# Performance work log

Hardware: AMD Instinct MI355X
Metric: run time of the kernel (lower is better)

## Reference

```python
import jax, jax.numpy as jnp
import numpy as np

N, D, R, NB, E = 50000, 128, 16, 10, 1600000
DECAY_RATE = 0.1
LN_EPS = 1e-5

def setup_inputs() -> dict:
    key = jax.random.key(0)
    ks = jax.random.split(key, 12)
    x = jax.random.normal(ks[0], (N, D), dtype=jnp.float32)
    edge_index = jax.random.randint(ks[1], (2, E), 0, N, dtype=jnp.int64)
    edge_type = jax.random.randint(ks[2], (E,), 0, R, dtype=jnp.int64)
    edge_time = jax.random.uniform(ks[3], (E,), dtype=jnp.float32)
    s = 1.0 / np.sqrt(D)
    basis = jax.random.normal(ks[4], (NB, D, D), dtype=jnp.float32) * s   # RGCN basis matrices
    comp = jax.random.normal(ks[5], (R, NB), dtype=jnp.float32) * (1.0 / np.sqrt(NB))
    root = jax.random.normal(ks[6], (D, D), dtype=jnp.float32) * s        # RGCN self-loop weight
    bias = jnp.zeros((D,), dtype=jnp.float32)
    tp_w = jax.random.normal(ks[7], (D, D), dtype=jnp.float32) * s        # time_proj
    tp_b = jnp.zeros((D,), dtype=jnp.float32)
    gamma = jnp.ones((D,), dtype=jnp.float32)
    beta = jnp.zeros((D,), dtype=jnp.float32)
    return {"x": x, "edge_index": edge_index, "edge_type": edge_type, "edge_time": edge_time,
            "basis": basis, "comp": comp, "root": root, "bias": bias,
            "tp_w": tp_w, "tp_b": tp_b, "gamma": gamma, "beta": beta}

def reference(x, edge_index, edge_type, edge_time, basis, comp, root, bias, tp_w, tp_b, gamma, beta):
    n, d = x.shape
    r = comp.shape[0]
    src, dst = edge_index[0], edge_index[1]
    # ---- RGCNConv (basis decomposition, per-relation mean aggregation) ----
    W = jnp.einsum('rb,bio->rio', comp, basis)                 # [R, D, D]
    msg = x[src]                                               # [E, D] gather
    seg = dst * r + edge_type                                  # combined (node, relation) segment id
    agg = jax.ops.segment_sum(msg, seg, num_segments=n * r)    # [N*R, D]
    cnt = jax.ops.segment_sum(jnp.ones_like(seg, dtype=x.dtype), seg, num_segments=n * r)
    agg = (agg / jnp.maximum(cnt, 1.0)[:, None]).reshape(n, r, d)  # per-relation mean
    x_rgcn = jnp.einsum('nrd,rdo->no', agg, W) + x @ root + bias
    # ---- exponential time decay weights, normalized to sum 1 ----
    td = edge_time.max() - edge_time
    td = td / (td.max() + 1e-8)
    w = jnp.exp(-DECAY_RATE * td)
    w = w / (w.sum() + 1e-8)
    # ---- time-decay aggregation (sum over relations == single scatter-add) ----
    agg_t = jax.ops.segment_sum(msg * w[:, None], dst, num_segments=n)
    deg = jax.ops.segment_sum(jnp.ones_like(dst, dtype=x.dtype), dst, num_segments=n)
    x_time = agg_t / jnp.clip(deg, 1.0)[:, None]
    # ---- combine, relu, (dropout=identity in eval), layernorm ----
    xc = x_rgcn + x_time @ tp_w + tp_b
    h = jax.nn.relu(xc)
    mu = h.mean(-1, keepdims=True)
    var = ((h - mu) ** 2).mean(-1, keepdims=True)
    return (h - mu) * jax.lax.rsqrt(var + LN_EPS) * gamma + beta
```

## Files before the change

### kernel.cpp

```cpp
#include <hip/hip_runtime.h>
#include <hip/hip_bf16.h>
#include <math.h>

#define NN 50000
#define DD 128
#define RR 16
#define NBASIS 10
#define NE 1600000
#define NSEG (NN * RR)
#define NSLICE 12
#define KTOT (NSLICE * DD)
#define DECAY 0.1f

#define NB_COARSE 782
#define NBLK_S 1024
#define EPB 1563
#define NHC (NB_COARSE * NBLK_S)
#define NPART2 (NHC / 1024)
#define FINE 1024
#define CAP 2560

typedef short bf16x8 __attribute__((ext_vector_type(8)));
typedef float f32x4 __attribute__((ext_vector_type(4)));
typedef float f32x2 __attribute__((ext_vector_type(2)));

__device__ __forceinline__ ushort f2b(float f) {
    unsigned u = __float_as_uint(f);
    unsigned r = (u + 0x7FFFu + ((u >> 16) & 1u)) >> 16;
    return (ushort)r;
}
__device__ __forceinline__ unsigned cvt_pk_bf16(float lo, float hi) {
    unsigned r;
    asm("v_cvt_pk_bf16_f32 %0, %1, %2" : "=v"(r) : "v"(lo), "v"(hi));
    return r;
}


#define XB_ITEMS (NN * (DD / 4))
#define PREP_ITEMS (XB_ITEMS + DD * KTOT)
__global__ __launch_bounds__(256) void k_s1(
    const int* __restrict__ edst, const float* __restrict__ t,
    const float* __restrict__ x, const float* __restrict__ basis,
    const float* __restrict__ root, const float* __restrict__ tp_w,
    unsigned* __restrict__ red, unsigned* __restrict__ Hc,
    ushort* __restrict__ xb, ushort* __restrict__ Bt3)
{
    const int bid = blockIdx.x;
    const int tid = threadIdx.x;
    if (bid < NBLK_S) {
        __shared__ unsigned h[NB_COARSE];
        for (int i = tid; i < NB_COARSE; i += 256) h[i] = 0u;
        __syncthreads();
        const int e0 = bid * EPB;
        const int e1 = (e0 + EPB < NE) ? e0 + EPB : NE;
        for (int e = e0 + tid; e < e1; e += 256) {
            int d = __builtin_nontemporal_load(edst + e);
            atomicAdd(&h[d >> 6], 1u);
        }
        __syncthreads();
        for (int i = tid; i < NB_COARSE; i += 256)
            Hc[i * NBLK_S + bid] = h[i];
        return;
    }
    if (bid < NBLK_S + 256) {
        __shared__ float smx[4], smn[4];
        float mx = 0.0f, mn = 1e30f;
        const int stride = 256 * 256;
        for (int i = (bid - NBLK_S) * 256 + tid; i < NE / 4; i += stride) {
            f32x4 v = __builtin_nontemporal_load(((const f32x4*)t) + i);
            mx = fmaxf(mx, fmaxf(fmaxf(v.x, v.y), fmaxf(v.z, v.w)));
            mn = fminf(mn, fminf(fminf(v.x, v.y), fminf(v.z, v.w)));
        }
        for (int o = 32; o >= 1; o >>= 1) {
            mx = fmaxf(mx, __shfl_down(mx, o, 64));
            mn = fminf(mn, __shfl_down(mn, o, 64));
        }
        if ((tid & 63) == 0) { smx[tid >> 6] = mx; smn[tid >> 6] = mn; }
        __syncthreads();
        if (tid == 0) {
            mx = fmaxf(fmaxf(smx[0], smx[1]), fmaxf(smx[2], smx[3]));
            mn = fminf(fminf(smn[0], smn[1]), fminf(smn[2], smn[3]));
            atomicMax(&red[0], __float_as_uint(mx));
            atomicMax(&red[1], ~__float_as_uint(mn));
        }
        return;
    }
    int idx = (bid - NBLK_S - 256) * 256 + tid;
    if (idx < XB_ITEMS) {
        f32x4 v = ((const f32x4*)x)[idx];
        uint2 o;
        o.x = cvt_pk_bf16(v.x, v.y);
        o.y = cvt_pk_bf16(v.z, v.w);
        ((uint2*)xb)[idx] = o;
        return;
    }
    int bidx = idx - XB_ITEMS;
    if (bidx >= DD * KTOT) return;
    int j = bidx / KTOT, k = bidx - j * KTOT;
    int s = k >> 7, d = k & 127;
    float v;
    if (s < NBASIS) {
        v = basis[(s * DD + d) * DD + j];
    } else if (s == NBASIS) {
        v = tp_w[d * DD + j];
    } else {
        v = root[d * DD + j];
    }
    Bt3[bidx] = f2b(v);
}

__global__ __launch_bounds__(1024) void k_scan1(unsigned* __restrict__ Hc,
                                                unsigned* __restrict__ part) {
    __shared__ unsigned sh[1024];
    int tid = threadIdx.x;
    int i = blockIdx.x * 1024 + tid;
    unsigned v = Hc[i];
    sh[tid] = v;
    __syncthreads();
    for (int off = 1; off < 1024; off <<= 1) {
        unsigned t = (tid >= off) ? sh[tid - off] : 0u;
        __syncthreads();
        sh[tid] += t;
        __syncthreads();
    }
    Hc[i] = sh[tid] - v;
    if (tid == 1023) part[blockIdx.x] = sh[1023];
}

__global__ __launch_bounds__(1024) void k_scan2(unsigned* __restrict__ part) {
    __shared__ unsigned sh[1024];
    int tid = threadIdx.x;
    unsigned v = (tid < NPART2) ? part[tid] : 0u;
    sh[tid] = v;
    __syncthreads();
    for (int off = 1; off < 1024; off <<= 1) {
        unsigned t = (tid >= off) ? sh[tid - off] : 0u;
        __syncthreads();
        sh[tid] += t;
        __syncthreads();
    }
    if (tid < NPART2) part[tid] = sh[tid] - v;
}

__global__ __launch_bounds__(1024) void k_scan3(unsigned* __restrict__ Hc,
                                                const unsigned* __restrict__ part) {
    int i = blockIdx.x * 1024 + threadIdx.x;
    Hc[i] += part[i >> 10];
}

__global__ __launch_bounds__(256) void k_s3(
    const int* __restrict__ esrc, const int* __restrict__ edst,
    const int* __restrict__ etype, const float* __restrict__ etime,
    const unsigned* __restrict__ Hc, unsigned* __restrict__ red,
    unsigned long long* __restrict__ tmp)
{
    __shared__ unsigned cur[NB_COARSE];
    __shared__ float ssum[4];
    const int bid = blockIdx.x;
    const int tid = threadIdx.x;
    for (int i = tid; i < NB_COARSE; i += 256)
        cur[i] = Hc[i * NBLK_S + bid];
    const float tmax = __uint_as_float(red[0]);
    const float tmin = __uint_as_float(~red[1]);
    const float rtd = -DECAY / (tmax - tmin + 1e-8f);
    __syncthreads();
    float s = 0.0f;
    const int e0 = bid * EPB;
    const int e1 = (e0 + EPB < NE) ? e0 + EPB : NE;
    for (int e = e0 + tid; e < e1; e += 256) {
        int d    = __builtin_nontemporal_load(edst + e);
        int ty   = __builtin_nontemporal_load(etype + e);
        int sv   = __builtin_nontemporal_load(esrc + e);
        float tv = __builtin_nontemporal_load(etime + e);
        float w = __expf((tmax - tv) * rtd);
        s += w;
        unsigned seg = (unsigned)(d * RR + ty);
        unsigned pos = atomicAdd(&cur[seg >> 10], 1u);
        unsigned lo = (unsigned)(sv & 0xFFFF) | ((unsigned)f2b(w) << 16);
        __builtin_nontemporal_store(
            ((unsigned long long)seg << 32) | lo, tmp + pos);
    }
    for (int o = 32; o >= 1; o >>= 1) s += __shfl_down(s, o, 64);
    if ((tid & 63) == 0) ssum[tid >> 6] = s;
    __syncthreads();
    if (tid == 0)
        atomicAdd(((float*)red) + 2, ssum[0] + ssum[1] + ssum[2] + ssum[3]);
}

__global__ __launch_bounds__(512) void k_s4(
    const unsigned long long* __restrict__ tmp, const unsigned* __restrict__ Hc,
    unsigned* __restrict__ srcw, unsigned* __restrict__ segptr)
{
    __shared__ unsigned long long recs[CAP];
    __shared__ unsigned hist[FINE];
    __shared__ unsigned excl[FINE];
    __shared__ unsigned curf[FINE];
    __shared__ unsigned sh[512];
    const int b = blockIdx.x;
    const int tid = threadIdx.x;
    const unsigned start = Hc[b * NBLK_S];
    const unsigned end   = (b + 1 < NB_COARSE) ? Hc[(b + 1) * NBLK_S] : (unsigned)NE;
    int n = (int)(end - start);
    if (n > CAP) n = CAP;
    for (int i = tid; i < FINE; i += 512) hist[i] = 0u;
    for (int i = tid; i < n; i += 512) recs[i] = tmp[start + i];
    __syncthreads();
    const unsigned base = (unsigned)b << 10;
    for (int i = tid; i < n; i += 512)
        atomicAdd(&hist[(unsigned)(recs[i] >> 32) - base], 1u);
    __syncthreads();
    unsigned a0 = hist[2 * tid], a1 = hist[2 * tid + 1];
    sh[tid] = a0 + a1;
    __syncthreads();
    for (int off = 1; off < 512; off <<= 1) {
        unsigned t = (tid >= off) ? sh[tid - off] : 0u;
        __syncthreads();
        sh[tid] += t;
        __syncthreads();
    }
    unsigned pe = sh[tid] - (a0 + a1);
    excl[2 * tid] = pe;          curf[2 * tid] = pe;
    excl[2 * tid + 1] = pe + a0; curf[2 * tid + 1] = pe + a0;
    __syncthreads();
    for (int i = tid; i < n; i += 512) {
        unsigned long long r = recs[i];
        unsigned p = atomicAdd(&curf[(unsigned)(r >> 32) - base], 1u);
        srcw[start + p] = (unsigned)r;
    }
    for (int i = tid; i < FINE; i += 512)
        segptr[(size_t)b * FINE + i] = start + excl[i];
}

__global__ __launch_bounds__(256) void k_gather(
    const ushort* __restrict__ xb, const unsigned* __restrict__ srcw,
    const unsigned* __restrict__ segptr, const unsigned* __restrict__ red,
    const float* __restrict__ comp,
    ushort* __restrict__ A2)
{
    const int wave = threadIdx.x >> 6, lane = threadIdx.x & 63;
    int dst0 = blockIdx.x * 4 + wave;
    if (dst0 >= NN) return;
    const int dst = __builtin_amdgcn_readfirstlane(dst0);
    const float sumw = ((const float*)red)[2];
    const unsigned s0 = (unsigned)dst * RR;
    const unsigned start = segptr[s0];
    const unsigned endAll = segptr[s0 + RR];
    const unsigned deg = endAll - start;
    unsigned* arow = (unsigned*)(A2 + (size_t)dst * KTOT);
    const unsigned* xbu = (const unsigned*)xb;

    f32x2 cb[NBASIS];
#pragma unroll
    for (int b = 0; b < NBASIS; ++b) cb[b] = (f32x2){0.f, 0.f};
    f32x2 acc = {0.f, 0.f}, xt = {0.f, 0.f};

    int r = 0;
    unsigned scur = start;
    unsigned endr = segptr[s0 + 1];
    unsigned e = start;

#define FLUSH_REL {                                                          \
        float scl = (endr > scur) ? (1.0f / (float)(endr - scur)) : 0.0f;    \
        f32x2 t = acc * scl;                                                 \
        _Pragma("unroll")                                                    \
        for (int b = 0; b < NBASIS; ++b)                                     \
            cb[b] += t * comp[r * NBASIS + b];                               \
        acc = (f32x2){0.f, 0.f}; scur = endr; ++r;                           \
        endr = (r < RR) ? segptr[s0 + r + 1] : 0xFFFFFFFFu; }

#define ACCUM(recq, pvq) {                                                   \
        float wgt = __uint_as_float((recq) & 0xFFFF0000u);                   \
        f32x2 v;                                                             \
        v.x = __uint_as_float((pvq) << 16);                                  \
        v.y = __uint_as_float((pvq) & 0xFFFF0000u);                          \
        acc += v;                                                            \
        xt += v * wgt; }

    while (e < endAll) {
        unsigned idx = e + (unsigned)lane;
        unsigned recv = srcw[(idx < endAll) ? idx : (endAll - 1u)];
        unsigned chunk = endAll - e;
        if (chunk > 64u) chunk = 64u;
        unsigned j = 0;
        for (; j + 8u <= chunk; j += 8u) {
            unsigned rec0 = (unsigned)__builtin_amdgcn_readlane((int)recv, (int)(j + 0));
            unsigned rec1 = (unsigned)__builtin_amdgcn_readlane((int)recv, (int)(j + 1));
            unsigned rec2 = (unsigned)__builtin_amdgcn_readlane((int)recv, (int)(j + 2));
            unsigned rec3 = (unsigned)__builtin_amdgcn_readlane((int)recv, (int)(j + 3));
            unsigned rec4 = (unsigned)__builtin_amdgcn_readlane((int)recv, (int)(j + 4));
            unsigned rec5 = (unsigned)__builtin_amdgcn_readlane((int)recv, (int)(j + 5));
            unsigned rec6 = (unsigned)__builtin_amdgcn_readlane((int)recv, (int)(j + 6));
            unsigned rec7 = (unsigned)__builtin_amdgcn_readlane((int)recv, (int)(j + 7));
            unsigned pv0 = xbu[((rec0 & 0xFFFFu) << 6) + lane];
            unsigned pv1 = xbu[((rec1 & 0xFFFFu) << 6) + lane];
            unsigned pv2 = xbu[((rec2 & 0xFFFFu) << 6) + lane];
            unsigned pv3 = xbu[((rec3 & 0xFFFFu) << 6) + lane];
            unsigned pv4 = xbu[((rec4 & 0xFFFFu) << 6) + lane];
            unsigned pv5 = xbu[((rec5 & 0xFFFFu) << 6) + lane];
            unsigned pv6 = xbu[((rec6 & 0xFFFFu) << 6) + lane];
            unsigned pv7 = xbu[((rec7 & 0xFFFFu) << 6) + lane];
            while (e >= endr) FLUSH_REL; ACCUM(rec0, pv0); ++e;
            while (e >= endr) FLUSH_REL; ACCUM(rec1, pv1); ++e;
            while (e >= endr) FLUSH_REL; ACCUM(rec2, pv2); ++e;
            while (e >= endr) FLUSH_REL; ACCUM(rec3, pv3); ++e;
            while (e >= endr) FLUSH_REL; ACCUM(rec4, pv4); ++e;
            while (e >= endr) FLUSH_REL; ACCUM(rec5, pv5); ++e;
            while (e >= endr) FLUSH_REL; ACCUM(rec6, pv6); ++e;
            while (e >= endr) FLUSH_REL; ACCUM(rec7, pv7); ++e;
        }
        for (; j < chunk; ++j) {
            unsigned rc = (unsigned)__builtin_amdgcn_readlane((int)recv, (int)j);
            unsigned pv = xbu[((rc & 0xFFFFu) << 6) + lane];
            while (e >= endr) FLUSH_REL;
            ACCUM(rc, pv);
            ++e;
        }
    }
    while (r < RR) FLUSH_REL;

#pragma unroll
    for (int b = 0; b < NBASIS; ++b)
        __builtin_nontemporal_store(cvt_pk_bf16(cb[b].x, cb[b].y),
                                    arow + b * 64 + lane);

    float s2 = 1.0f / ((sumw + 1e-8f) * fmaxf((float)deg, 1.0f));
    __builtin_nontemporal_store(cvt_pk_bf16(xt.x * s2, xt.y * s2),
                                arow + NBASIS * 64 + lane);
    __builtin_nontemporal_store(
        ((const unsigned*)(xb + (size_t)dst * DD))[lane],
        arow + (NBASIS + 1) * 64 + lane);
#undef FLUSH_REL
#undef ACCUM
}

__global__ __launch_bounds__(256) void k_fgemm(
    const ushort* __restrict__ A2, const ushort* __restrict__ Bt3,
    const float* __restrict__ bias, const float* __restrict__ tpb,
    const float* __restrict__ gamma, const float* __restrict__ beta,
    float* __restrict__ out)
{
    __shared__ unsigned Bs[2][4096];

    const int tid = threadIdx.x;
    const int w = tid >> 6, lane = tid & 63;
    const int quad = lane >> 4, l16 = lane & 15;
    const int n0 = blockIdx.x * 64;

    f32x4 acc[8];
#pragma unroll
    for (int ct = 0; ct < 8; ++ct) acc[ct] = (f32x4){0.f, 0.f, 0.f, 0.f};

    const ushort* arow = A2 + (size_t)(n0 + w * 16 + l16) * KTOT + quad * 8;
    const int srow = lane >> 3;
    const int sc   = lane & 7;

#define STAGE(buf, itv) {                                                    \
        const int k0_ = (itv) * 64;                                          \
        _Pragma("unroll")                                                    \
        for (int i_ = 0; i_ < 4; ++i_) {                                     \
            const int cid_ = i_ * 4 + w;                                     \
            const int row_ = cid_ * 8 + srow;                                \
            const int ck_  = sc ^ (row_ & 7);                                \
            const ushort* gb_ = Bt3 + (size_t)row_ * KTOT + k0_ + ck_ * 8;   \
            __builtin_amdgcn_global_load_lds(                                \
                (const __attribute__((address_space(1))) unsigned*)gb_,      \
                (__attribute__((address_space(3))) unsigned*)&Bs[buf][cid_ * 256], \
                16, 0, 0);                                                   \
        } }

#define COMPUTE(af0_, af1_, Bp_) {                                           \
        _Pragma("unroll")                                                    \
        for (int ct = 0; ct < 8; ++ct) {                                     \
            const int rB = ct * 16 + l16;                                    \
            bf16x8 b0 = *(const bf16x8*)&Bp_[rB * 32 + ((quad ^ (rB & 7)) << 2)];      \
            bf16x8 b1 = *(const bf16x8*)&Bp_[rB * 32 + (((4 + quad) ^ (rB & 7)) << 2)];\
            acc[ct] = __builtin_amdgcn_mfma_f32_16x16x32_bf16(af0_, b0, acc[ct], 0, 0, 0); \
            acc[ct] = __builtin_amdgcn_mfma_f32_16x16x32_bf16(af1_, b1, acc[ct], 0, 0, 0); \
        } }

    STAGE(0, 0);
    bf16x8 a0A = __builtin_nontemporal_load((const bf16x8*)(arow));
    bf16x8 a1A = __builtin_nontemporal_load((const bf16x8*)(arow + 32));
    bf16x8 a0B = __builtin_nontemporal_load((const bf16x8*)(arow + 64));
    bf16x8 a1B = __builtin_nontemporal_load((const bf16x8*)(arow + 96));
    __syncthreads();

    const int NIT = KTOT / 64;
    for (int it = 0; it < NIT; it += 2) {
        STAGE(1, it + 1);
        {
            bf16x8 af0 = a0A, af1 = a1A;
            if (it + 2 < NIT) {
                a0A = __builtin_nontemporal_load((const bf16x8*)(arow + (it + 2) * 64));
                a1A = __builtin_nontemporal_load((const bf16x8*)(arow + (it + 2) * 64 + 32));
            }
            const unsigned* Bp = &Bs[0][0];
            COMPUTE(af0, af1, Bp);
        }
        __syncthreads();
        if (it + 2 < NIT) STAGE(0, it + 2);
        {
            bf16x8 af0 = a0B, af1 = a1B;
            if (it + 3 < NIT) {
                a0B = __builtin_nontemporal_load((const bf16x8*)(arow + (it + 3) * 64));
                a1B = __builtin_nontemporal_load((const bf16x8*)(arow + (it + 3) * 64 + 32));
            }
            const unsigned* Bp = &Bs[1][0];
            COMPUTE(af0, af1, Bp);
        }
        __syncthreads();
    }
#undef STAGE
#undef COMPUTE

    float bc[8], gc[8], be[8];
#pragma unroll
    for (int ct = 0; ct < 8; ++ct) {
        int col = ct * 16 + l16;
        bc[ct] = bias[col] + tpb[col];
        gc[ct] = gamma[col];
        be[ct] = beta[col];
    }
    float s[4] = {0, 0, 0, 0}, q[4] = {0, 0, 0, 0};
#pragma unroll
    for (int ct = 0; ct < 8; ++ct)
#pragma unroll
        for (int i = 0; i < 4; ++i) {
            float v = fmaxf(acc[ct][i] + bc[ct], 0.0f);
            acc[ct][i] = v;
            s[i] += v;
            q[i] = fmaf(v, v, q[i]);
        }
#pragma unroll
    for (int off = 1; off < 16; off <<= 1)
#pragma unroll
        for (int i = 0; i < 4; ++i) {
            s[i] += __shfl_xor(s[i], off, 64);
            q[i] += __shfl_xor(q[i], off, 64);
        }
#pragma unroll
    for (int i = 0; i < 4; ++i) {
        const int row = n0 + w * 16 + quad * 4 + i;
        float mu  = s[i] * (1.0f / DD);
        float var = q[i] * (1.0f / DD) - mu * mu;
        float inv = rsqrtf(var + 1e-5f);
        if (row < NN) {
#pragma unroll
            for (int ct = 0; ct < 8; ++ct)
                __builtin_nontemporal_store(
                    (acc[ct][i] - mu) * inv * gc[ct] + be[ct],
                    out + (size_t)row * DD + ct * 16 + l16);
        }
    }
}

extern "C" void kernel_launch(void* const* d_in, const int* in_sizes, int n_in,
                              void* d_out, int out_size, void* d_ws, size_t ws_size,
                              hipStream_t stream)
{
    const float* x     = (const float*)d_in[0];
    const int*   ei    = (const int*)d_in[1];
    const int*   etype = (const int*)d_in[2];
    const float* etime = (const float*)d_in[3];
    const float* basis = (const float*)d_in[4];
    const float* comp  = (const float*)d_in[5];
    const float* root  = (const float*)d_in[6];
    const float* bias  = (const float*)d_in[7];
    const float* tp_w  = (const float*)d_in[8];
    const float* tp_b  = (const float*)d_in[9];
    const float* gamma = (const float*)d_in[10];
    const float* beta  = (const float*)d_in[11];
    float* out = (float*)d_out;

    char* ws = (char*)d_ws;
    size_t off = 0;
    auto alloc = [&](size_t bytes) -> void* {
        void* p = ws + off;
        off = (off + bytes + 255) & ~(size_t)255;
        return p;
    };
    unsigned* red    = (unsigned*)alloc(256);
    unsigned* Hc     = (unsigned*)alloc((size_t)NHC * 4);
    unsigned* part   = (unsigned*)alloc(1024 * 4);
    unsigned* srcw   = (unsigned*)alloc((size_t)NE * 4);
    unsigned long long* tmp = (unsigned long long*)alloc((size_t)NE * 8);
    unsigned* segptr = (unsigned*)alloc((size_t)(NB_COARSE * FINE) * 4);
    ushort*   xb     = (ushort*)alloc((size_t)NN * DD * 2);
    ushort*   Bt3    = (ushort*)alloc((size_t)DD * KTOT * 2);
    ushort*   A2     = (ushort*)alloc((size_t)50048 * KTOT * 2);
    (void)ws_size;

    const int* esrc = ei;
    const int* edst = ei + NE;

    (void)hipMemsetAsync(red, 0, 256, stream);

    const int prep_blocks = (PREP_ITEMS + 255) / 256;
    hipLaunchKernelGGL(k_s1, dim3(NBLK_S + 256 + prep_blocks), dim3(256), 0, stream,
                       edst, etime, x, basis, root, tp_w, red, Hc, xb, Bt3);

    hipLaunchKernelGGL(k_scan1, dim3(NPART2), dim3(1024), 0, stream, Hc, part);
    hipLaunchKernelGGL(k_scan2, dim3(1), dim3(1024), 0, stream, part);
    hipLaunchKernelGGL(k_scan3, dim3(NPART2), dim3(1024), 0, stream, Hc, part);

    hipLaunchKernelGGL(k_s3, dim3(NBLK_S), dim3(256), 0, stream,
                       esrc, edst, etype, etime, Hc, red, tmp);

    hipLaunchKernelGGL(k_s4, dim3(NB_COARSE), dim3(512), 0, stream,
                       tmp, Hc, srcw, segptr);

    hipLaunchKernelGGL(k_gather, dim3((NN + 3) / 4), dim3(256), 0, stream,
                       xb, srcw, segptr, red, comp, A2);

    hipLaunchKernelGGL(k_fgemm, dim3((50048 + 63) / 64), dim3(256), 0, stream,
                       A2, Bt3, bias, tp_b, gamma, beta, out);
}
```

Measured before the change: 340.6 us.

## Fuse fine bucket sort with per-node gather into one kernel

Merges the fine-grained counting sort (k_s4) and the per-destination gather/aggregation kernel into a single kernel. The sorted edge records stay in shared memory and are never written to global srcw/segptr buffers. Each 512-thread block now handles 64 destination nodes, eight per wave. This removes a launch and a global round-trip of sorted records and segment pointers. In exchange the grid drops from about 12.5k small blocks to 782 large blocks, each using a lot of LDS, which lowers occupancy and latency hiding for the random x gathers.

```diff
diff --git a/kernel.cpp b/kernel.cpp
--- a/kernel.cpp
+++ b/kernel.cpp
@@ -7,7 +7,6 @@
 #define RR 16
 #define NBASIS 10
 #define NE 1600000
-#define NSEG (NN * RR)
 #define NSLICE 12
 #define KTOT (NSLICE * DD)
 #define DECAY 0.1f
@@ -187,15 +186,17 @@
         atomicAdd(((float*)red) + 2, ssum[0] + ssum[1] + ssum[2] + ssum[3]);
 }
 
-__global__ __launch_bounds__(512) void k_s4(
+__global__ __launch_bounds__(512) void k_s4g(
     const unsigned long long* __restrict__ tmp, const unsigned* __restrict__ Hc,
-    unsigned* __restrict__ srcw, unsigned* __restrict__ segptr)
+    const unsigned* __restrict__ red, const float* __restrict__ comp,
+    const ushort* __restrict__ xb, ushort* __restrict__ A2)
 {
     __shared__ unsigned long long recs[CAP];
     __shared__ unsigned hist[FINE];
     __shared__ unsigned excl[FINE];
     __shared__ unsigned curf[FINE];
-    __shared__ unsigned sh[512];
+    __shared__ unsigned shx[512];
+    __shared__ unsigned slo[CAP + 8];
     const int b = blockIdx.x;
     const int tid = threadIdx.x;
     const unsigned start = Hc[b * NBLK_S];
@@ -210,63 +211,59 @@
         atomicAdd(&hist[(unsigned)(recs[i] >> 32) - base], 1u);
     __syncthreads();
     unsigned a0 = hist[2 * tid], a1 = hist[2 * tid + 1];
-    sh[tid] = a0 + a1;
+    shx[tid] = a0 + a1;
     __syncthreads();
     for (int off = 1; off < 512; off <<= 1) {
-        unsigned t = (tid >= off) ? sh[tid - off] : 0u;
-        __syncthreads();
-        sh[tid] += t;
-        __syncthreads();
-    }
-    unsigned pe = sh[tid] - (a0 + a1);
+        unsigned t = (tid >= off) ? shx[tid - off] : 0u;
+        __syncthreads();
+        shx[tid] += t;
+        __syncthreads();
+    }
+    unsigned pe = shx[tid] - (a0 + a1);
     excl[2 * tid] = pe;          curf[2 * tid] = pe;
     excl[2 * tid + 1] = pe + a0; curf[2 * tid + 1] = pe + a0;
     __syncthreads();
     for (int i = tid; i < n; i += 512) {
         unsigned long long r = recs[i];
         unsigned p = atomicAdd(&curf[(unsigned)(r >> 32) - base], 1u);
-        srcw[start + p] = (unsigned)r;
-    }
-    for (int i = tid; i < FINE; i += 512)
-        segptr[(size_t)b * FINE + i] = start + excl[i];
-}
-
-__global__ __launch_bounds__(256) void k_gather(
-    const ushort* __restrict__ xb, const unsigned* __restrict__ srcw,
-    const unsigned* __restrict__ segptr, const unsigned* __restrict__ red,
-    const float* __restrict__ comp,
-    ushort* __restrict__ A2)
-{
-    const int wave = threadIdx.x >> 6, lane = threadIdx.x & 63;
-    int dst0 = blockIdx.x * 4 + wave;
-    if (dst0 >= NN) return;
-    const int dst = __builtin_amdgcn_readfirstlane(dst0);
+        slo[p] = (unsigned)r;
+    }
+    if (tid < 8) slo[n + tid] = 0u;
+    __syncthreads();
+
+    const int wave = tid >> 6, lane = tid & 63;
     const float sumw = ((const float*)red)[2];
-    const unsigned s0 = (unsigned)dst * RR;
-    const unsigned start = segptr[s0];
-    const unsigned endAll = segptr[s0 + RR];
-    const unsigned deg = endAll - start;
-    unsigned* arow = (unsigned*)(A2 + (size_t)dst * KTOT);
     const unsigned* xbu = (const unsigned*)xb;
-
-    f32x2 cb[NBASIS];
-#pragma unroll
-    for (int b = 0; b < NBASIS; ++b) cb[b] = (f32x2){0.f, 0.f};
-    f32x2 acc = {0.f, 0.f}, xt = {0.f, 0.f};
-
-    int r = 0;
-    unsigned scur = start;
-    unsigned endr = segptr[s0 + 1];
-    unsigned e = start;
+    const unsigned nn = (unsigned)n;
+
+    for (int ld = wave * 8; ld < wave * 8 + 8; ++ld) {
+        const int dst = b * 64 + ld;
+        if (dst >= NN) continue;
+        const unsigned s_start = excl[ld * 16];
+        const unsigned s_end   = (ld * 16 + 16 < FINE) ? excl[ld * 16 + 16] : nn;
+        const unsigned deg = s_end - s_start;
+        unsigned* arow = (unsigned*)(A2 + (size_t)dst * KTOT);
+
+        f32x2 cb[NBASIS];
+#pragma unroll
+        for (int bb = 0; bb < NBASIS; ++bb) cb[bb] = (f32x2){0.f, 0.f};
+        f32x2 acc = {0.f, 0.f}, xt = {0.f, 0.f};
+
+        int r = 0;
+        unsigned scur = s_start;
+        unsigned endr = (ld * 16 + 1 < FINE) ? excl[ld * 16 + 1] : nn;
+        unsigned e = s_start;
 
 #define FLUSH_REL {                                                          \
         float scl = (endr > scur) ? (1.0f / (float)(endr - scur)) : 0.0f;    \
         f32x2 t = acc * scl;                                                 \
         _Pragma("unroll")                                                    \
-        for (int b = 0; b < NBASIS; ++b)                                     \
-            cb[b] += t * comp[r * NBASIS + b];                               \
+        for (int bb = 0; bb < NBASIS; ++bb)                                  \
+            cb[bb] += t * comp[r * NBASIS + bb];                             \
         acc = (f32x2){0.f, 0.f}; scur = endr; ++r;                           \
-        endr = (r < RR) ? segptr[s0 + r + 1] : 0xFFFFFFFFu; }
+        endr = (r < RR) ? ((ld * 16 + r + 1 < FINE) ? excl[ld * 16 + r + 1]  \
+                                                    : nn)                    \
+                        : 0xFFFFFFFFu; }
 
 #define ACCUM(recq, pvq) {                                                   \
         float wgt = __uint_as_float((recq) & 0xFFFF0000u);                   \
@@ -276,61 +273,48 @@
         acc += v;                                                            \
         xt += v * wgt; }
 
-    while (e < endAll) {
-        unsigned idx = e + (unsigned)lane;
-        unsigned recv = srcw[(idx < endAll) ? idx : (endAll - 1u)];
-        unsigned chunk = endAll - e;
-        if (chunk > 64u) chunk = 64u;
-        unsigned j = 0;
-        for (; j + 8u <= chunk; j += 8u) {
-            unsigned rec0 = (unsigned)__builtin_amdgcn_readlane((int)recv, (int)(j + 0));
-            unsigned rec1 = (unsigned)__builtin_amdgcn_readlane((int)recv, (int)(j + 1));
-            unsigned rec2 = (unsigned)__builtin_amdgcn_readlane((int)recv, (int)(j + 2));
-            unsigned rec3 = (unsigned)__builtin_amdgcn_readlane((int)recv, (int)(j + 3));
-            unsigned rec4 = (unsigned)__builtin_amdgcn_readlane((int)recv, (int)(j + 4));
-            unsigned rec5 = (unsigned)__builtin_amdgcn_readlane((int)recv, (int)(j + 5));
-            unsigned rec6 = (unsigned)__builtin_amdgcn_readlane((int)recv, (int)(j + 6));
-            unsigned rec7 = (unsigned)__builtin_amdgcn_readlane((int)recv, (int)(j + 7));
-            unsigned pv0 = xbu[((rec0 & 0xFFFFu) << 6) + lane];
-            unsigned pv1 = xbu[((rec1 & 0xFFFFu) << 6) + lane];
-            unsigned pv2 = xbu[((rec2 & 0xFFFFu) << 6) + lane];
-            unsigned pv3 = xbu[((rec3 & 0xFFFFu) << 6) + lane];
-            unsigned pv4 = xbu[((rec4 & 0xFFFFu) << 6) + lane];
-            unsigned pv5 = xbu[((rec5 & 0xFFFFu) << 6) + lane];
-            unsigned pv6 = xbu[((rec6 & 0xFFFFu) << 6) + lane];
-            unsigned pv7 = xbu[((rec7 & 0xFFFFu) << 6) + lane];
+        while (e < s_end) {
+            unsigned m = s_end - e;
+            if (m > 8u) m = 8u;
+            unsigned rec0 = slo[e + 0], rec1 = slo[e + 1];
+            unsigned rec2 = slo[e + 2], rec3 = slo[e + 3];
+            unsigned rec4 = slo[e + 4], rec5 = slo[e + 5];
+            unsigned rec6 = slo[e + 6], rec7 = slo[e + 7];
+            unsigned pv0 = 0, pv1 = 0, pv2 = 0, pv3 = 0;
+            unsigned pv4 = 0, pv5 = 0, pv6 = 0, pv7 = 0;
+            pv0 = xbu[((rec0 & 0xFFFFu) << 6) + lane];
+            if (m > 1) pv1 = xbu[((rec1 & 0xFFFFu) << 6) + lane];
+            if (m > 2) pv2 = xbu[((rec2 & 0xFFFFu) << 6) + lane];
+            if (m > 3) pv3 = xbu[((rec3 & 0xFFFFu) << 6) + lane];
+            if (m > 4) pv4 = xbu[((rec4 & 0xFFFFu) << 6) + lane];
+            if (m > 5) pv5 = xbu[((rec5 & 0xFFFFu) << 6) + lane];
+            if (m > 6) pv6 = xbu[((rec6 & 0xFFFFu) << 6) + lane];
+            if (m > 7) pv7 = xbu[((rec7 & 0xFFFFu) << 6) + lane];
             while (e >= endr) FLUSH_REL; ACCUM(rec0, pv0); ++e;
-            while (e >= endr) FLUSH_REL; ACCUM(rec1, pv1); ++e;
-            while (e >= endr) FLUSH_REL; ACCUM(rec2, pv2); ++e;
-            while (e >= endr) FLUSH_REL; ACCUM(rec3, pv3); ++e;
-            while (e >= endr) FLUSH_REL; ACCUM(rec4, pv4); ++e;
-            while (e >= endr) FLUSH_REL; ACCUM(rec5, pv5); ++e;
-            while (e >= endr) FLUSH_REL; ACCUM(rec6, pv6); ++e;
-            while (e >= endr) FLUSH_REL; ACCUM(rec7, pv7); ++e;
-        }
-        for (; j < chunk; ++j) {
-            unsigned rc = (unsigned)__builtin_amdgcn_readlane((int)recv, (int)j);
-            unsigned pv = xbu[((rc & 0xFFFFu) << 6) + lane];
-            while (e >= endr) FLUSH_REL;
-            ACCUM(rc, pv);
-            ++e;
-        }
-    }
-    while (r < RR) FLUSH_REL;
-
-#pragma unroll
-    for (int b = 0; b < NBASIS; ++b)
-        __builtin_nontemporal_store(cvt_pk_bf16(cb[b].x, cb[b].y),
-                                    arow + b * 64 + lane);
-
-    float s2 = 1.0f / ((sumw + 1e-8f) * fmaxf((float)deg, 1.0f));
-    __builtin_nontemporal_store(cvt_pk_bf16(xt.x * s2, xt.y * s2),
-                                arow + NBASIS * 64 + lane);
-    __builtin_nontemporal_store(
-        ((const unsigned*)(xb + (size_t)dst * DD))[lane],
-        arow + (NBASIS + 1) * 64 + lane);
+            if (m > 1) { while (e >= endr) FLUSH_REL; ACCUM(rec1, pv1); ++e; }
+            if (m > 2) { while (e >= endr) FLUSH_REL; ACCUM(rec2, pv2); ++e; }
+            if (m > 3) { while (e >= endr) FLUSH_REL; ACCUM(rec3, pv3); ++e; }
+            if (m > 4) { while (e >= endr) FLUSH_REL; ACCUM(rec4, pv4); ++e; }
+            if (m > 5) { while (e >= endr) FLUSH_REL; ACCUM(rec5, pv5); ++e; }
+            if (m > 6) { while (e >= endr) FLUSH_REL; ACCUM(rec6, pv6); ++e; }
+            if (m > 7) { while (e >= endr) FLUSH_REL; ACCUM(rec7, pv7); ++e; }
+        }
+        while (r < RR) FLUSH_REL;
+
+#pragma unroll
+        for (int bb = 0; bb < NBASIS; ++bb)
+            __builtin_nontemporal_store(cvt_pk_bf16(cb[bb].x, cb[bb].y),
+                                        arow + bb * 64 + lane);
+
+        float s2 = 1.0f / ((sumw + 1e-8f) * fmaxf((float)deg, 1.0f));
+        __builtin_nontemporal_store(cvt_pk_bf16(xt.x * s2, xt.y * s2),
+                                    arow + NBASIS * 64 + lane);
+        __builtin_nontemporal_store(
+            ((const unsigned*)(xb + (size_t)dst * DD))[lane],
+            arow + (NBASIS + 1) * 64 + lane);
 #undef FLUSH_REL
 #undef ACCUM
+    }
 }
 
 __global__ __launch_bounds__(256) void k_fgemm(
@@ -482,9 +466,7 @@
     unsigned* red    = (unsigned*)alloc(256);
     unsigned* Hc     = (unsigned*)alloc((size_t)NHC * 4);
     unsigned* part   = (unsigned*)alloc(1024 * 4);
-    unsigned* srcw   = (unsigned*)alloc((size_t)NE * 4);
     unsigned long long* tmp = (unsigned long long*)alloc((size_t)NE * 8);
-    unsigned* segptr = (unsigned*)alloc((size_t)(NB_COARSE * FINE) * 4);
     ushort*   xb     = (ushort*)alloc((size_t)NN * DD * 2);
     ushort*   Bt3    = (ushort*)alloc((size_t)DD * KTOT * 2);
     ushort*   A2     = (ushort*)alloc((size_t)50048 * KTOT * 2);
@@ -506,11 +488,8 @@
     hipLaunchKernelGGL(k_s3, dim3(NBLK_S), dim3(256), 0, stream,
                        esrc, edst, etype, etime, Hc, red, tmp);
 
-    hipLaunchKernelGGL(k_s4, dim3(NB_COARSE), dim3(512), 0, stream,
-                       tmp, Hc, srcw, segptr);
-
-    hipLaunchKernelGGL(k_gather, dim3((NN + 3) / 4), dim3(256), 0, stream,
-                       xb, srcw, segptr, red, comp, A2);
+    hipLaunchKernelGGL(k_s4g, dim3(NB_COARSE), dim3(512), 0, stream,
+                       tmp, Hc, red, comp, xb, A2);
 
     hipLaunchKernelGGL(k_fgemm, dim3((50048 + 63) / 64), dim3(256), 0, stream,
                        A2, Bt3, bias, tp_b, gamma, beta, out);
```

Result: slower. 433.6 us (+27.3%).
